# Performance work log

Hardware: AMD Instinct MI355X
Metric: run time of the kernel (lower is better)

## Reference

```python
import jax, jax.numpy as jnp
import numpy as np

V, D, H_FF, NH, L = 32000, 1024, 4096, 16, 4
HD = D // NH  # 64
B, T = 2, 2048
EPS = 1e-6
ROPE_BASE = 10000.0


def setup_inputs() -> dict:
    key = jax.random.key(0)
    ks = jax.random.split(key, 16)
    s = 0.02
    inp = {
        "idx": jax.random.randint(ks[0], (B, T), 0, V, dtype=jnp.int32),
        "targets": jax.random.randint(ks[1], (B, T), 0, V, dtype=jnp.int32),
        "embed": jax.random.normal(ks[2], (V, D), jnp.float32) * s,
        "wq": jax.random.normal(ks[3], (L, D, D), jnp.float32) * s,
        "wk": jax.random.normal(ks[4], (L, D, D), jnp.float32) * s,
        "wv": jax.random.normal(ks[5], (L, D, D), jnp.float32) * s,
        "wo": jax.random.normal(ks[6], (L, D, D), jnp.float32) * s,
        "w_gate": jax.random.normal(ks[7], (L, D, H_FF), jnp.float32) * s,
        "w_up": jax.random.normal(ks[8], (L, D, H_FF), jnp.float32) * s,
        "w_down": jax.random.normal(ks[9], (L, H_FF, D), jnp.float32) * s,
        "attn_norm": jnp.ones((L, D), jnp.float32),
        "mlp_norm": jnp.ones((L, D), jnp.float32),
        "final_norm": jnp.ones((D,), jnp.float32),
        "lm_head": jax.random.normal(ks[10], (V, D), jnp.float32) * s,
    }
    return inp


def rms_norm(x, w):
    var = jnp.mean(jnp.square(x), axis=-1, keepdims=True)
    return x * jax.lax.rsqrt(var + EPS) * w


def make_rope(t_len, hd):
    inv_freq = 1.0 / (ROPE_BASE ** (jnp.arange(0, hd, 2, dtype=jnp.float32) / hd))
    angles = jnp.arange(t_len, dtype=jnp.float32)[:, None] * inv_freq[None, :]  # [T, HD/2]
    return jnp.cos(angles), jnp.sin(angles)


def apply_rope(x, cos, sin):
    # x: [B, T, NH, HD]; half-split rotation (HF Llama style)
    x1, x2 = jnp.split(x, 2, axis=-1)
    c = cos[None, :, None, :]
    s = sin[None, :, None, :]
    return jnp.concatenate([x1 * c - x2 * s, x2 * c + x1 * s], axis=-1)


def forward(idx, targets, embed, wq, wk, wv, wo, w_gate, w_up, w_down,
            attn_norm, mlp_norm, final_norm, lm_head):
    b, t_len = idx.shape
    x = embed[idx]  # [B, T, D]
    cos, sin = make_rope(t_len, HD)
    causal = jnp.tril(jnp.ones((t_len, t_len), dtype=bool))
    scale = 1.0 / np.sqrt(HD)
    for l in range(L):
        # attention
        h = rms_norm(x, attn_norm[l])
        q = (h @ wq[l]).reshape(b, t_len, NH, HD)
        k = (h @ wk[l]).reshape(b, t_len, NH, HD)
        v = (h @ wv[l]).reshape(b, t_len, NH, HD)
        q = apply_rope(q, cos, sin)
        k = apply_rope(k, cos, sin)
        scores = jnp.einsum('bqhd,bkhd->bhqk', q, k) * scale
        scores = jnp.where(causal[None, None], scores, -jnp.inf)
        attn = jax.nn.softmax(scores, axis=-1)
        o = jnp.einsum('bhqk,bkhd->bqhd', attn, v).reshape(b, t_len, D)
        x = x + o @ wo[l]
        # SwiGLU MLP
        h = rms_norm(x, mlp_norm[l])
        x = x + (jax.nn.silu(h @ w_gate[l]) * (h @ w_up[l])) @ w_down[l]
    x = rms_norm(x, final_norm)
    logits = jnp.einsum('btd,vd->btv', x, lm_head)  # [B, T, V]
    logp = jax.nn.log_softmax(logits, axis=-1)
    nll = -jnp.take_along_axis(logp, targets[..., None], axis=-1)[..., 0]
    loss = jnp.mean(nll)
    return logits, loss


def reference(idx, targets, embed, wq, wk, wv, wo, w_gate, w_up, w_down,
              attn_norm, mlp_norm, final_norm, lm_head):
    return forward(idx, targets, embed, wq, wk, wv, wo, w_gate, w_up, w_down,
                   attn_norm, mlp_norm, final_norm, lm_head)
```

## Files before the change

kernel.cpp:

```cpp
#include <hip/hip_runtime.h>

typedef __attribute__((ext_vector_type(8))) short short8;
typedef __attribute__((ext_vector_type(4))) float f32x4;
typedef __attribute__((ext_vector_type(8))) unsigned short u16x8;
typedef unsigned short u16;

#define V_SIZE 32000
#define D_MODEL 1024
#define HFF 4096
#define NHEAD 16
#define HDIM 64
#define NLAYER 4
#define BT 4096
#define TSEQ 2048
#define QKV_STRIDE 3072
#define GU_STRIDE 8192

__device__ __forceinline__ u16 f2bf(float f) {
  union { float f; unsigned u; } v; v.f = f;
  unsigned r = v.u + 0x7fffu + ((v.u >> 16) & 1u);
  return (u16)(r >> 16);
}
__device__ __forceinline__ float bf2f(u16 h) {
  union { unsigned u; float f; } v; v.u = ((unsigned)h) << 16;
  return v.f;
}

__device__ __forceinline__ void gload_lds16(const void* g, void* l) {
  __builtin_amdgcn_global_load_lds((__attribute__((address_space(1))) void*)g,
                                   (__attribute__((address_space(3))) void*)l, 16, 0, 0);
}


__global__ void rope_table_kernel(float* __restrict__ cosb, float* __restrict__ sinb) {
  int i = blockIdx.x * 256 + threadIdx.x;
  int t = i >> 5, fi = i & 31;
  float freq = exp2f(-(2.0f * (float)fi / 64.0f) * log2f(10000.0f));
  float ang = (float)t * freq;
  cosb[i] = cosf(ang);
  sinb[i] = sinf(ang);
}

__global__ void convert_bf16_kernel(const float* __restrict__ src, u16* __restrict__ dst,
                                    const float* __restrict__ fn, long n8) {
  long i = (long)blockIdx.x * 256 + threadIdx.x;
  long stride = (long)gridDim.x * 256;
  for (; i < n8; i += stride) {
    const float4* s = (const float4*)(src + i * 8);
    float4 a = s[0], b = s[1];
    int k0 = (int)((i * 8) & (D_MODEL - 1));
    u16x8 r;
    r[0] = f2bf(a.x * fn[k0 + 0]); r[1] = f2bf(a.y * fn[k0 + 1]);
    r[2] = f2bf(a.z * fn[k0 + 2]); r[3] = f2bf(a.w * fn[k0 + 3]);
    r[4] = f2bf(b.x * fn[k0 + 4]); r[5] = f2bf(b.y * fn[k0 + 5]);
    r[6] = f2bf(b.z * fn[k0 + 6]); r[7] = f2bf(b.w * fn[k0 + 7]);
    *(u16x8*)(dst + i * 8) = r;
  }
}

__global__ __launch_bounds__(256) void transpose_bf16_kernel(const float* __restrict__ src0,
                                                             u16* __restrict__ dst0, int R, int C,
                                                             long srcStride, long dstStride,
                                                             int rowMode,
                                                             const float* __restrict__ nw0,
                                                             int nwStride) {
  __shared__ float tile[32][33];
  const float* src = src0 + (size_t)blockIdx.z * srcStride;
  u16* dst = dst0 + (size_t)blockIdx.z * dstStride;
  const float* nw = nw0 ? nw0 + (size_t)blockIdx.z * nwStride : nullptr;
  int tx = threadIdx.x & 31, ty = threadIdx.x >> 5;
  int bx = blockIdx.x, by = blockIdx.y;
#pragma unroll
  for (int i = 0; i < 32; i += 8) {
    int r = by * 32 + ty + i, c = bx * 32 + tx;
    tile[ty + i][tx] = src[(size_t)r * C + c];
  }
  __syncthreads();
#pragma unroll
  for (int i = 0; i < 32; i += 8) {
    int c = bx * 32 + ty + i;
    int r = by * 32 + tx;
    float val = tile[tx][ty + i];
    if (nw) val *= nw[r];
    int drow = c;
    if (rowMode == 1) drow = ((c >> 6) << 7) | (c & 63);
    else if (rowMode == 2) drow = ((c >> 6) << 7) | 64 | (c & 63);
    dst[(size_t)drow * R + r] = f2bf(val);
  }
}

__global__ __launch_bounds__(256) void embed_gather_kernel(const int* __restrict__ idx,
                                                           const float* __restrict__ embed,
                                                           float* __restrict__ x,
                                                           u16* __restrict__ xb,
                                                           float* __restrict__ rinv) {
  int t = blockIdx.x;
  int id = idx[t];
  float4 v = ((const float4*)embed)[(size_t)id * 256 + threadIdx.x];
  ((float4*)x)[(size_t)t * 256 + threadIdx.x] = v;
  u16* hp = xb + (size_t)t * D_MODEL + threadIdx.x * 4;
  hp[0] = f2bf(v.x); hp[1] = f2bf(v.y); hp[2] = f2bf(v.z); hp[3] = f2bf(v.w);
  float ss = v.x * v.x + v.y * v.y + v.z * v.z + v.w * v.w;
#pragma unroll
  for (int m = 32; m > 0; m >>= 1) ss += __shfl_xor(ss, m, 64);
  __shared__ float wsum[4];
  if ((threadIdx.x & 63) == 0) wsum[threadIdx.x >> 6] = ss;
  __syncthreads();
  if (threadIdx.x == 0) {
    float tot = wsum[0] + wsum[1] + wsum[2] + wsum[3];
    rinv[t] = rsqrtf(tot * (1.0f / (float)D_MODEL) + 1e-6f);
  }
}

__global__ void rinv_kernel(const float* __restrict__ ssqPart, float* __restrict__ rinv) {
  int r = blockIdx.x * 256 + threadIdx.x;
  float s = 0.f;
#pragma unroll
  for (int i = 0; i < 16; i++) s += ssqPart[(size_t)r * 16 + i];
  rinv[r] = rsqrtf(s * (1.0f / (float)D_MODEL) + 1e-6f);
}

__global__ void scale_xb_kernel(const u16* __restrict__ xb, const float* __restrict__ rinv,
                                u16* __restrict__ xbf) {
  long i = (long)blockIdx.x * 256 + threadIdx.x;
  int row = (int)(i >> 7);
  float ri = rinv[row];
  short8 v = *(const short8*)(xb + i * 8);
  u16x8 r;
#pragma unroll
  for (int j = 0; j < 8; j++) r[j] = f2bf(bf2f((u16)v[j]) * ri);
  *(u16x8*)(xbf + i * 8) = r;
}

__global__ __launch_bounds__(256) void vtrans_kernel(const u16* __restrict__ qkv,
                                                     u16* __restrict__ vt) {
  __shared__ u16 lds[64 * 64];
  const int tid = threadIdx.x;
  const int bh = blockIdx.y, tt = blockIdx.x;
  const int b = bh >> 4, h = bh & 15;
  const int tok0 = b * TSEQ + tt * 64;
  const int hoff = 2 * D_MODEL + h * HDIM;
#pragma unroll
  for (int it = 0; it < 2; it++) {
    int idx = it * 256 + tid;
    int row = idx >> 3, c = (idx & 7) * 8;
    short8 v = *(const short8*)(qkv + (size_t)(tok0 + row) * QKV_STRIDE + hoff + c);
    *(short8*)&lds[row * 64 + (c ^ ((row & 7) << 3))] = v;
  }
  __syncthreads();
#pragma unroll
  for (int it = 0; it < 2; it++) {
    int idx = it * 256 + tid;
    int d = idx >> 3, t0 = (idx & 7) * 8;
    u16x8 pk;
#pragma unroll
    for (int j = 0; j < 8; j++) {
      int t = t0 + j;
      pk[j] = lds[t * 64 + (((d & ~7) ^ ((t & 7) << 3)) | (d & 7))];
    }
    *(u16x8*)(vt + ((size_t)bh * 64 + d) * TSEQ + tt * 64 + t0) = pk;
  }
}

template <int EPI>
__global__ __launch_bounds__(256, 4) void gemm128_kernel(const u16* __restrict__ A,
                                                         const u16* __restrict__ B, void* Cp,
                                                         float* __restrict__ partM,
                                                         float* __restrict__ partS,
                                                         const float* __restrict__ cosb,
                                                         const float* __restrict__ sinb,
                                                         const float* __restrict__ rinv,
                                                         int M, int N, int K, int chunkBn) {
  __shared__ __align__(16) u16 smem_ab[2][128 * 64];
  u16* As = smem_ab[0];
  u16* Bs = smem_ab[1];
  const int tid = threadIdx.x;
  const int lane = tid & 63, wid = tid >> 6;
  const int wr = wid >> 1, wc = wid & 1;
  const int q = lane >> 4, l15 = lane & 15;
  const int nbm = M >> 7;
  const int nbmx = nbm >> 3;
  const int cs = nbm * chunkBn;
  const int chunk = (int)blockIdx.x / cs;
  const int r0 = (int)blockIdx.x - chunk * cs;
  const int s2 = r0 >> 3;
  const int bm = (r0 & 7) * nbmx + (s2 % nbmx);
  const int bn = chunk * chunkBn + (s2 / nbmx);
  const size_t abase = (size_t)bm * 128 * K;
  const size_t bbase = (size_t)bn * 128 * K;
  f32x4 acc[4][4] = {};
  for (int k0 = 0; k0 < K; k0 += 64) {
#pragma unroll
    for (int i = 0; i < 4; i++) {
      int idx8 = i * 256 + tid;
      int row = idx8 >> 3, ch = idx8 & 7;
      int sc = (ch ^ (row & 7)) << 3;
      gload_lds16(A + abase + (size_t)row * K + k0 + sc, As + idx8 * 8);
      gload_lds16(B + bbase + (size_t)row * K + k0 + sc, Bs + idx8 * 8);
    }
    __syncthreads();
#pragma unroll
    for (int ks = 0; ks < 2; ks++) {
      short8 af[4], bfr[4];
      int chunkc = ks * 4 + q;
#pragma unroll
      for (int mi = 0; mi < 4; mi++) {
        int row = wr * 64 + mi * 16 + l15;
        af[mi] = *(const short8*)&As[row * 64 + ((chunkc ^ (row & 7)) << 3)];
      }
#pragma unroll
      for (int ni = 0; ni < 4; ni++) {
        int row = wc * 64 + ni * 16 + l15;
        bfr[ni] = *(const short8*)&Bs[row * 64 + ((chunkc ^ (row & 7)) << 3)];
      }
#pragma unroll
      for (int mi = 0; mi < 4; mi++)
#pragma unroll
        for (int ni = 0; ni < 4; ni++)
          acc[mi][ni] = __builtin_amdgcn_mfma_f32_16x16x32_bf16(af[mi], bfr[ni], acc[mi][ni], 0, 0, 0);
    }
    __syncthreads();
  }

  if (EPI == 5) {
    float* upf = (float*)&smem_ab[0][0];
    if (wc == 1) {
#pragma unroll
      for (int mi = 0; mi < 4; mi++)
#pragma unroll
        for (int ni = 0; ni < 4; ni++)
#pragma unroll
          for (int j = 0; j < 4; j++) {
            int r = wr * 64 + mi * 16 + q * 4 + j;
            int cswz = (ni ^ ((r >> 2) & 3)) * 16 + l15;
            upf[r * 64 + cswz] = acc[mi][ni][j];
          }
    }
    __syncthreads();
    if (wc == 0) {
#pragma unroll
      for (int mi = 0; mi < 4; mi++)
#pragma unroll
        for (int j = 0; j < 4; j++) {
          int rloc = wr * 64 + mi * 16 + q * 4 + j;
          int rr = bm * 128 + rloc;
          float ri = rinv[rr];
#pragma unroll
          for (int ni = 0; ni < 4; ni++) {
            int cswz = (ni ^ ((rloc >> 2) & 3)) * 16 + l15;
            float g = acc[mi][ni][j] * ri;
            float u = upf[rloc * 64 + cswz] * ri;
            float rsl = g / (1.0f + expf(-g)) * u;
            ((u16*)Cp)[(size_t)rr * (N >> 1) + bn * 64 + ni * 16 + l15] = f2bf(rsl);
          }
        }
    }
    return;
  }

#pragma unroll
  for (int mi = 0; mi < 4; mi++)
#pragma unroll
    for (int j = 0; j < 4; j++) {
      int rr = bm * 128 + wr * 64 + mi * 16 + q * 4 + j;
      float vv[4];
      if (EPI == 4) {
        float ri = rinv[rr];
#pragma unroll
        for (int ni = 0; ni < 4; ni++) vv[ni] = acc[mi][ni][j] * ri;
      } else {
#pragma unroll
        for (int ni = 0; ni < 4; ni++) vv[ni] = acc[mi][ni][j];
      }
      if (EPI == 0) {
        float mx = fmaxf(fmaxf(vv[0], vv[1]), fmaxf(vv[2], vv[3]));
        mx = fmaxf(mx, __shfl_xor(mx, 1, 64));
        mx = fmaxf(mx, __shfl_xor(mx, 2, 64));
        mx = fmaxf(mx, __shfl_xor(mx, 4, 64));
        mx = fmaxf(mx, __shfl_xor(mx, 8, 64));
        float sm = 0.f;
#pragma unroll
        for (int ni = 0; ni < 4; ni++) sm += expf(vv[ni] - mx);
        sm += __shfl_xor(sm, 1, 64);
        sm += __shfl_xor(sm, 2, 64);
        sm += __shfl_xor(sm, 4, 64);
        sm += __shfl_xor(sm, 8, 64);
        if (l15 == 0) {
          int nt = (N >> 6);
          partM[(size_t)rr * nt + (bn << 1) + wc] = mx;
          partS[(size_t)rr * nt + (bn << 1) + wc] = sm;
        }
      }
      if (EPI == 4) {
        if (((bn << 1) + wc) < 32) {
          int t = rr & (TSEQ - 1);
#pragma unroll
          for (int ni = 0; ni < 2; ni++) {
            int fi = ni * 16 + l15;
            float c = cosb[t * 32 + fi], s = sinb[t * 32 + fi];
            float x1 = vv[ni], x2 = vv[ni + 2];
            vv[ni] = x1 * c - x2 * s;
            vv[ni + 2] = x2 * c + x1 * s;
          }
        }
      }
#pragma unroll
      for (int ni = 0; ni < 4; ni++) {
        int cn = bn * 128 + wc * 64 + ni * 16 + l15;
        size_t off = (size_t)rr * N + cn;
        if (EPI == 0) __builtin_nontemporal_store(vv[ni], (float*)Cp + off);
        else ((u16*)Cp)[off] = f2bf(vv[ni]);
      }
    }
}

__global__ __launch_bounds__(256, 4) void gemm64_kernel(const u16* __restrict__ A,
                                                        const u16* __restrict__ B, float* __restrict__ Cp,
                                                        const float* __restrict__ resid,
                                                        u16* __restrict__ xbout,
                                                        float* __restrict__ ssqPart,
                                                        int M, int N, int K) {
  __shared__ __align__(16) u16 As[64 * 64];
  __shared__ __align__(16) u16 Bs[128 * 64];
  const int tid = threadIdx.x;
  const int lane = tid & 63, wid = tid >> 6;
  const int wr = wid >> 1, wc = wid & 1;
  const int q = lane >> 4, l15 = lane & 15;
  const int nbm = M >> 6;
  const int nbmx = nbm >> 3;
  const int s2 = (int)blockIdx.x >> 3;
  const int bm = ((int)blockIdx.x & 7) * nbmx + (s2 % nbmx);
  const int bn = s2 / nbmx;
  const size_t abase = (size_t)bm * 64 * K;
  const size_t bbase = (size_t)bn * 128 * K;
  f32x4 acc[2][4] = {};
  for (int k0 = 0; k0 < K; k0 += 64) {
#pragma unroll
    for (int i = 0; i < 2; i++) {
      int idx8 = i * 256 + tid;
      int row = idx8 >> 3, ch = idx8 & 7;
      int sc = (ch ^ (row & 7)) << 3;
      gload_lds16(A + abase + (size_t)row * K + k0 + sc, As + idx8 * 8);
    }
#pragma unroll
    for (int i = 0; i < 4; i++) {
      int idx8 = i * 256 + tid;
      int row = idx8 >> 3, ch = idx8 & 7;
      int sc = (ch ^ (row & 7)) << 3;
      gload_lds16(B + bbase + (size_t)row * K + k0 + sc, Bs + idx8 * 8);
    }
    __syncthreads();
#pragma unroll
    for (int ks = 0; ks < 2; ks++) {
      short8 af[2], bfr[4];
      int chunkc = ks * 4 + q;
#pragma unroll
      for (int mi = 0; mi < 2; mi++) {
        int row = wr * 32 + mi * 16 + l15;
        af[mi] = *(const short8*)&As[row * 64 + ((chunkc ^ (row & 7)) << 3)];
      }
#pragma unroll
      for (int ni = 0; ni < 4; ni++) {
        int row = wc * 64 + ni * 16 + l15;
        bfr[ni] = *(const short8*)&Bs[row * 64 + ((chunkc ^ (row & 7)) << 3)];
      }
#pragma unroll
      for (int mi = 0; mi < 2; mi++)
#pragma unroll
        for (int ni = 0; ni < 4; ni++)
          acc[mi][ni] = __builtin_amdgcn_mfma_f32_16x16x32_bf16(af[mi], bfr[ni], acc[mi][ni], 0, 0, 0);
    }
    __syncthreads();
  }
#pragma unroll
  for (int mi = 0; mi < 2; mi++)
#pragma unroll
    for (int j = 0; j < 4; j++) {
      int rr = bm * 64 + wr * 32 + mi * 16 + q * 4 + j;
      float ssq = 0.f;
#pragma unroll
      for (int ni = 0; ni < 4; ni++) {
        int cn = bn * 128 + wc * 64 + ni * 16 + l15;
        size_t off = (size_t)rr * N + cn;
        float nx = resid[off] + acc[mi][ni][j];
        Cp[off] = nx;
        xbout[off] = f2bf(nx);
        ssq += nx * nx;
      }
      ssq += __shfl_xor(ssq, 1, 64);
      ssq += __shfl_xor(ssq, 2, 64);
      ssq += __shfl_xor(ssq, 4, 64);
      ssq += __shfl_xor(ssq, 8, 64);
      if (l15 == 0) ssqPart[(size_t)rr * 16 + (bn << 1) + wc] = ssq;
    }
}

__global__ __launch_bounds__(256) void attn_kernel(const u16* __restrict__ qkv,
                                                   const u16* __restrict__ vt,
                                                   u16* __restrict__ o) {
  __shared__ __align__(16) u16 Ks[64 * 64];
  __shared__ __align__(16) u16 Vt[64 * 64];
  __shared__ u16 Ps[4][16 * 64];
  const u16* q = qkv;
  const u16* k = qkv + D_MODEL;
  const int tid = threadIdx.x, lane = tid & 63, wid = tid >> 6;
  const int qg = lane >> 4, l15 = lane & 15;
  const int bh = blockIdx.y;
  const int b = bh >> 4, h = bh & 15;
  const int tok0 = b * TSEQ;
  const int hoff = h * HDIM;
  const u16* vtb = vt + (size_t)bh * 64 * TSEQ;

  for (int half = 0; half < 2; half++) {
    const int qt = half == 0 ? (int)blockIdx.x : 31 - (int)blockIdx.x;
    const int qrow0 = qt * 64 + wid * 16;

    short8 aq[2];
#pragma unroll
    for (int ks = 0; ks < 2; ks++) {
      int r = qrow0 + l15;
      int d = ks * 32 + qg * 8;
      aq[ks] = *(const short8*)(q + (size_t)(tok0 + r) * QKV_STRIDE + hoff + d);
    }
    f32x4 oacc[4] = {};
    float mrow[4], lrow[4];
#pragma unroll
    for (int j = 0; j < 4; j++) { mrow[j] = -1e30f; lrow[j] = 0.f; }

    const int nkt = qt + 1;
    for (int kt = 0; kt < nkt; kt++) {
      const int kv0 = kt * 64;
#pragma unroll
      for (int it = 0; it < 2; it++) {
        int idx = it * 256 + tid;
        int row = idx >> 3, ch = idx & 7;
        int sc = (ch ^ (row & 7)) << 3;
        gload_lds16(k + (size_t)(tok0 + kv0 + row) * QKV_STRIDE + hoff + sc, Ks + idx * 8);
        gload_lds16(vtb + (size_t)row * TSEQ + kv0 + sc, Vt + idx * 8);
      }
      __syncthreads();
      f32x4 sc[4] = {};
#pragma unroll
      for (int ks = 0; ks < 2; ks++) {
        short8 bk[4];
        int kcol = ks * 32 + qg * 8;
#pragma unroll
        for (int ni = 0; ni < 4; ni++) {
          int r = ni * 16 + l15;
          bk[ni] = *(const short8*)&Ks[r * 64 + (kcol ^ ((r & 7) << 3))];
        }
#pragma unroll
        for (int ni = 0; ni < 4; ni++)
          sc[ni] = __builtin_amdgcn_mfma_f32_16x16x32_bf16(aq[ks], bk[ni], sc[ni], 0, 0, 0);
      }
      float pm[4];
#pragma unroll
      for (int j = 0; j < 4; j++) pm[j] = -1e30f;
#pragma unroll
      for (int ni = 0; ni < 4; ni++)
#pragma unroll
        for (int j = 0; j < 4; j++) {
          int rq = qrow0 + qg * 4 + j;
          int ck = kv0 + ni * 16 + l15;
          float s = sc[ni][j] * 0.125f;
          if (ck > rq) s = -1e30f;
          sc[ni][j] = s;
          pm[j] = fmaxf(pm[j], s);
        }
#pragma unroll
      for (int j = 0; j < 4; j++) {
        float t = pm[j];
        t = fmaxf(t, __shfl_xor(t, 1, 64));
        t = fmaxf(t, __shfl_xor(t, 2, 64));
        t = fmaxf(t, __shfl_xor(t, 4, 64));
        t = fmaxf(t, __shfl_xor(t, 8, 64));
        pm[j] = t;
      }
#pragma unroll
      for (int j = 0; j < 4; j++) {
        float mn = fmaxf(mrow[j], pm[j]);
        float fac = expf(mrow[j] - mn);
        lrow[j] *= fac;
#pragma unroll
        for (int df = 0; df < 4; df++) oacc[df][j] *= fac;
        mrow[j] = mn;
      }
      float psum[4] = {};
#pragma unroll
      for (int ni = 0; ni < 4; ni++)
#pragma unroll
        for (int j = 0; j < 4; j++) {
          float p = expf(sc[ni][j] - mrow[j]);
          psum[j] += p;
          int r16 = qg * 4 + j;
          int cc = ni * 16 + l15;
          Ps[wid][r16 * 64 + (cc ^ ((r16 & 7) << 3))] = f2bf(p);
        }
#pragma unroll
      for (int j = 0; j < 4; j++) {
        float t = psum[j];
        t += __shfl_xor(t, 1, 64);
        t += __shfl_xor(t, 2, 64);
        t += __shfl_xor(t, 4, 64);
        t += __shfl_xor(t, 8, 64);
        lrow[j] += t;
      }
#pragma unroll
      for (int kf = 0; kf < 2; kf++) {
        short8 pa, bv[4];
        int kcol = kf * 32 + qg * 8;
        {
          int r = l15;
          pa = *(const short8*)&Ps[wid][r * 64 + (kcol ^ ((r & 7) << 3))];
        }
#pragma unroll
        for (int df = 0; df < 4; df++) {
          int r = df * 16 + l15;
          bv[df] = *(const short8*)&Vt[r * 64 + (kcol ^ ((r & 7) << 3))];
        }
#pragma unroll
        for (int df = 0; df < 4; df++)
          oacc[df] = __builtin_amdgcn_mfma_f32_16x16x32_bf16(pa, bv[df], oacc[df], 0, 0, 0);
      }
      __syncthreads();
    }
#pragma unroll
    for (int df = 0; df < 4; df++)
#pragma unroll
      for (int j = 0; j < 4; j++) {
        int r = qrow0 + qg * 4 + j;
        int d = df * 16 + l15;
        float val = oacc[df][j] / lrow[j];
        o[(size_t)(tok0 + r) * D_MODEL + hoff + d] = f2bf(val);
      }
  }
}


__global__ void nll_finalize_kernel(const float* __restrict__ partM, const float* __restrict__ partS,
                                    const float* __restrict__ logits, const int* __restrict__ targets,
                                    float* __restrict__ nll) {
  int tok = blockIdx.x;
  int lane = threadIdx.x;
  const int NTL = V_SIZE >> 6;
  float m = -1e30f, s = 0.f;
  for (int i = lane; i < NTL; i += 64) {
    float m2 = partM[(size_t)tok * NTL + i];
    float s2 = partS[(size_t)tok * NTL + i];
    float nm = fmaxf(m, m2);
    s = s * expf(m - nm) + s2 * expf(m2 - nm);
    m = nm;
  }
#pragma unroll
  for (int mask = 1; mask < 64; mask <<= 1) {
    float m2 = __shfl_xor(m, mask, 64);
    float s2 = __shfl_xor(s, mask, 64);
    float nm = fmaxf(m, m2);
    s = s * expf(m - nm) + s2 * expf(m2 - nm);
    m = nm;
  }
  if (lane == 0)
    nll[tok] = m + logf(s) - logits[(size_t)tok * V_SIZE + targets[tok]];
}

__global__ void loss_reduce_kernel(const float* __restrict__ nll, float* __restrict__ out) {
  float s = 0.f;
  for (int i = threadIdx.x; i < BT; i += 256) s += nll[i];
#pragma unroll
  for (int mask = 1; mask < 64; mask <<= 1) s += __shfl_xor(s, mask, 64);
  __shared__ float sm[4];
  if ((threadIdx.x & 63) == 0) sm[threadIdx.x >> 6] = s;
  __syncthreads();
  if (threadIdx.x == 0) out[0] = (sm[0] + sm[1] + sm[2] + sm[3]) / (float)BT;
}


extern "C" void kernel_launch(void* const* d_in, const int* in_sizes, int n_in,
                              void* d_out, int out_size, void* d_ws, size_t ws_size,
                              hipStream_t stream) {
  const int* idx = (const int*)d_in[0];
  const int* targets = (const int*)d_in[1];
  const float* embed = (const float*)d_in[2];
  const float* wq = (const float*)d_in[3];
  const float* wk = (const float*)d_in[4];
  const float* wv = (const float*)d_in[5];
  const float* wo = (const float*)d_in[6];
  const float* w_gate = (const float*)d_in[7];
  const float* w_up = (const float*)d_in[8];
  const float* w_down = (const float*)d_in[9];
  const float* attn_norm = (const float*)d_in[10];
  const float* mlp_norm = (const float*)d_in[11];
  const float* final_norm = (const float*)d_in[12];
  const float* lm_head = (const float*)d_in[13];
  float* out = (float*)d_out;

  char* ws = (char*)d_ws;
  size_t off = 0;
  auto alloc = [&](size_t bytes) {
    void* p = ws + off;
    off += (bytes + 255) & ~(size_t)255;
    return p;
  };
  const size_t DD = (size_t)D_MODEL * D_MODEL;
  float* rope_cos = (float*)alloc((size_t)TSEQ * 32 * 4);
  float* rope_sin = (float*)alloc((size_t)TSEQ * 32 * 4);
  float* X = (float*)alloc((size_t)BT * D_MODEL * 4);
  u16* Xb = (u16*)alloc((size_t)BT * D_MODEL * 2);
  u16* XbF = (u16*)alloc((size_t)BT * D_MODEL * 2);
  float* Rinv = (float*)alloc((size_t)BT * 4);
  float* SsqP = (float*)alloc((size_t)BT * 16 * 4);
  u16* QKVb = (u16*)alloc((size_t)BT * QKV_STRIDE * 2);
  u16* Vtb = (u16*)alloc((size_t)32 * 64 * TSEQ * 2);
  u16* Ob = (u16*)alloc((size_t)BT * D_MODEL * 2);
  u16* Gb = (u16*)alloc((size_t)BT * HFF * 2);
  u16* WQKVT = (u16*)alloc((size_t)NLAYER * QKV_STRIDE * D_MODEL * 2);
  u16* WOT = (u16*)alloc((size_t)NLAYER * DD * 2);
  u16* WGU = (u16*)alloc((size_t)NLAYER * GU_STRIDE * D_MODEL * 2);
  u16* WDT = (u16*)alloc((size_t)NLAYER * D_MODEL * HFF * 2);
  u16* LMH = (u16*)alloc((size_t)V_SIZE * D_MODEL * 2);
  float* NLLb = (float*)alloc((size_t)BT * 4);
  float* PartM = (float*)alloc((size_t)BT * (V_SIZE >> 6) * 4);
  float* PartS = (float*)alloc((size_t)BT * (V_SIZE >> 6) * 4);

  rope_table_kernel<<<256, 256, 0, stream>>>(rope_cos, rope_sin);
  convert_bf16_kernel<<<4096, 256, 0, stream>>>(lm_head, LMH, final_norm, (long)V_SIZE * D_MODEL / 8);
  embed_gather_kernel<<<BT, 256, 0, stream>>>(idx, embed, X, Xb, Rinv);

  const long QKVW = (long)QKV_STRIDE * D_MODEL;
  const long GUW = (long)GU_STRIDE * D_MODEL;
  const long DW = (long)D_MODEL * HFF;
  transpose_bf16_kernel<<<dim3(32, 32, NLAYER), 256, 0, stream>>>(wq, WQKVT, D_MODEL, D_MODEL, DD, QKVW, 0, attn_norm, D_MODEL);
  transpose_bf16_kernel<<<dim3(32, 32, NLAYER), 256, 0, stream>>>(wk, WQKVT + DD, D_MODEL, D_MODEL, DD, QKVW, 0, attn_norm, D_MODEL);
  transpose_bf16_kernel<<<dim3(32, 32, NLAYER), 256, 0, stream>>>(wv, WQKVT + 2 * DD, D_MODEL, D_MODEL, DD, QKVW, 0, attn_norm, D_MODEL);
  transpose_bf16_kernel<<<dim3(32, 32, NLAYER), 256, 0, stream>>>(wo, WOT, D_MODEL, D_MODEL, DD, DD, 0, nullptr, 0);
  transpose_bf16_kernel<<<dim3(128, 32, NLAYER), 256, 0, stream>>>(w_gate, WGU, D_MODEL, HFF, DW, GUW, 1, mlp_norm, D_MODEL);
  transpose_bf16_kernel<<<dim3(128, 32, NLAYER), 256, 0, stream>>>(w_up, WGU, D_MODEL, HFF, DW, GUW, 2, mlp_norm, D_MODEL);
  transpose_bf16_kernel<<<dim3(32, 128, NLAYER), 256, 0, stream>>>(w_down, WDT, HFF, D_MODEL, DW, DW, 0, nullptr, 0);

  for (int l = 0; l < NLAYER; l++) {
    gemm128_kernel<4><<<(QKV_STRIDE / 128) * (BT / 128), 256, 0, stream>>>(
        Xb, WQKVT + (size_t)l * QKVW, QKVb, nullptr, nullptr, rope_cos, rope_sin,
        Rinv, BT, QKV_STRIDE, D_MODEL, QKV_STRIDE / 128);
    vtrans_kernel<<<dim3(32, 32), 256, 0, stream>>>(QKVb, Vtb);
    attn_kernel<<<dim3(16, 32), 256, 0, stream>>>(QKVb, Vtb, Ob);
    gemm64_kernel<<<(BT / 64) * (D_MODEL / 128), 256, 0, stream>>>(
        Ob, WOT + (size_t)l * DD, X, X, Xb, SsqP, BT, D_MODEL, D_MODEL);
    rinv_kernel<<<BT / 256, 256, 0, stream>>>(SsqP, Rinv);

    gemm128_kernel<5><<<(GU_STRIDE / 128) * (BT / 128), 256, 0, stream>>>(
        Xb, WGU + (size_t)l * GUW, Gb, nullptr, nullptr, nullptr, nullptr,
        Rinv, BT, GU_STRIDE, D_MODEL, 32);
    gemm64_kernel<<<(BT / 64) * (D_MODEL / 128), 256, 0, stream>>>(
        Gb, WDT + (size_t)l * DW, X, X, Xb, SsqP, BT, D_MODEL, HFF);
    rinv_kernel<<<BT / 256, 256, 0, stream>>>(SsqP, Rinv);
  }

  scale_xb_kernel<<<BT * D_MODEL / (256 * 8), 256, 0, stream>>>(Xb, Rinv, XbF);
  gemm128_kernel<0><<<(V_SIZE / 128) * (BT / 128), 256, 0, stream>>>(
      XbF, LMH, out, PartM, PartS, nullptr, nullptr,
      nullptr, BT, V_SIZE, D_MODEL, 50);
  nll_finalize_kernel<<<BT, 64, 0, stream>>>(PartM, PartS, out, targets, NLLb);
  loss_reduce_kernel<<<1, 256, 0, stream>>>(NLLb, out + (size_t)BT * V_SIZE);
}
```

Before: 1.737 ms.

## Keep residual stream in bf16 and fold attention scale into Q projection

Removes the fp32 residual buffer X: the embed gather and residual GEMM epilogues now read and write only the bf16 Xb copy, so each residual GEMM avoids an fp32 read and write. The softmax scale and log2(e) are folded into the Q columns in the QKV epilogue, which lets attention use exp2f. Causal masking now runs only on the diagonal tile. Keeping the residual in bf16 adds rounding error that accumulates across layers and may threaten accuracy tolerance.

Measured after the change: 1.649 ms. 5.1% less time.

```diff
diff --git a/kernel.cpp b/kernel.cpp
--- a/kernel.cpp
+++ b/kernel.cpp
@@ -15,6 +15,7 @@
 #define TSEQ 2048
 #define QKV_STRIDE 3072
 #define GU_STRIDE 8192
+#define QSCALE 0.18033688011112043f
 
 __device__ __forceinline__ u16 f2bf(float f) {
   union { float f; unsigned u; } v; v.f = f;
@@ -91,13 +92,11 @@
 
 __global__ __launch_bounds__(256) void embed_gather_kernel(const int* __restrict__ idx,
                                                            const float* __restrict__ embed,
-                                                           float* __restrict__ x,
                                                            u16* __restrict__ xb,
                                                            float* __restrict__ rinv) {
   int t = blockIdx.x;
   int id = idx[t];
   float4 v = ((const float4*)embed)[(size_t)id * 256 + threadIdx.x];
-  ((float4*)x)[(size_t)t * 256 + threadIdx.x] = v;
   u16* hp = xb + (size_t)t * D_MODEL + threadIdx.x * 4;
   hp[0] = f2bf(v.x); hp[1] = f2bf(v.y); hp[2] = f2bf(v.z); hp[3] = f2bf(v.w);
   float ss = v.x * v.x + v.y * v.y + v.z * v.z + v.w * v.w;
@@ -266,6 +265,7 @@
       float vv[4];
       if (EPI == 4) {
         float ri = rinv[rr];
+        if (((bn << 1) + wc) < 16) ri *= QSCALE;
 #pragma unroll
         for (int ni = 0; ni < 4; ni++) vv[ni] = acc[mi][ni][j] * ri;
       } else {
@@ -315,8 +315,8 @@
 }
 
 __global__ __launch_bounds__(256, 4) void gemm64_kernel(const u16* __restrict__ A,
-                                                        const u16* __restrict__ B, float* __restrict__ Cp,
-                                                        const float* __restrict__ resid,
+                                                        const u16* __restrict__ B,
+                                                        const u16* __restrict__ resid,
                                                         u16* __restrict__ xbout,
                                                         float* __restrict__ ssqPart,
                                                         int M, int N, int K) {
@@ -382,8 +382,7 @@
       for (int ni = 0; ni < 4; ni++) {
         int cn = bn * 128 + wc * 64 + ni * 16 + l15;
         size_t off = (size_t)rr * N + cn;
-        float nx = resid[off] + acc[mi][ni][j];
-        Cp[off] = nx;
+        float nx = bf2f(resid[off]) + acc[mi][ni][j];
         xbout[off] = f2bf(nx);
         ssq += nx * nx;
       }
@@ -456,17 +455,24 @@
       float pm[4];
 #pragma unroll
       for (int j = 0; j < 4; j++) pm[j] = -1e30f;
-#pragma unroll
-      for (int ni = 0; ni < 4; ni++)
-#pragma unroll
-        for (int j = 0; j < 4; j++) {
-          int rq = qrow0 + qg * 4 + j;
-          int ck = kv0 + ni * 16 + l15;
-          float s = sc[ni][j] * 0.125f;
-          if (ck > rq) s = -1e30f;
-          sc[ni][j] = s;
-          pm[j] = fmaxf(pm[j], s);
-        }
+      if (kt == qt) {
+#pragma unroll
+        for (int ni = 0; ni < 4; ni++)
+#pragma unroll
+          for (int j = 0; j < 4; j++) {
+            int rq = qrow0 + qg * 4 + j;
+            int ck = kv0 + ni * 16 + l15;
+            float s = sc[ni][j];
+            if (ck > rq) s = -1e30f;
+            sc[ni][j] = s;
+            pm[j] = fmaxf(pm[j], s);
+          }
+      } else {
+#pragma unroll
+        for (int ni = 0; ni < 4; ni++)
+#pragma unroll
+          for (int j = 0; j < 4; j++) pm[j] = fmaxf(pm[j], sc[ni][j]);
+      }
 #pragma unroll
       for (int j = 0; j < 4; j++) {
         float t = pm[j];
@@ -479,7 +485,7 @@
 #pragma unroll
       for (int j = 0; j < 4; j++) {
         float mn = fmaxf(mrow[j], pm[j]);
-        float fac = expf(mrow[j] - mn);
+        float fac = exp2f(mrow[j] - mn);
         lrow[j] *= fac;
 #pragma unroll
         for (int df = 0; df < 4; df++) oacc[df][j] *= fac;
@@ -490,7 +496,7 @@
       for (int ni = 0; ni < 4; ni++)
 #pragma unroll
         for (int j = 0; j < 4; j++) {
-          float p = expf(sc[ni][j] - mrow[j]);
+          float p = exp2f(sc[ni][j] - mrow[j]);
           psum[j] += p;
           int r16 = qg * 4 + j;
           int cc = ni * 16 + l15;
@@ -604,7 +610,6 @@
   const size_t DD = (size_t)D_MODEL * D_MODEL;
   float* rope_cos = (float*)alloc((size_t)TSEQ * 32 * 4);
   float* rope_sin = (float*)alloc((size_t)TSEQ * 32 * 4);
-  float* X = (float*)alloc((size_t)BT * D_MODEL * 4);
   u16* Xb = (u16*)alloc((size_t)BT * D_MODEL * 2);
   u16* XbF = (u16*)alloc((size_t)BT * D_MODEL * 2);
   float* Rinv = (float*)alloc((size_t)BT * 4);
@@ -624,7 +629,7 @@
 
   rope_table_kernel<<<256, 256, 0, stream>>>(rope_cos, rope_sin);
   convert_bf16_kernel<<<4096, 256, 0, stream>>>(lm_head, LMH, final_norm, (long)V_SIZE * D_MODEL / 8);
-  embed_gather_kernel<<<BT, 256, 0, stream>>>(idx, embed, X, Xb, Rinv);
+  embed_gather_kernel<<<BT, 256, 0, stream>>>(idx, embed, Xb, Rinv);
 
   const long QKVW = (long)QKV_STRIDE * D_MODEL;
   const long GUW = (long)GU_STRIDE * D_MODEL;
@@ -644,14 +649,14 @@
     vtrans_kernel<<<dim3(32, 32), 256, 0, stream>>>(QKVb, Vtb);
     attn_kernel<<<dim3(16, 32), 256, 0, stream>>>(QKVb, Vtb, Ob);
     gemm64_kernel<<<(BT / 64) * (D_MODEL / 128), 256, 0, stream>>>(
-        Ob, WOT + (size_t)l * DD, X, X, Xb, SsqP, BT, D_MODEL, D_MODEL);
+        Ob, WOT + (size_t)l * DD, Xb, Xb, SsqP, BT, D_MODEL, D_MODEL);
     rinv_kernel<<<BT / 256, 256, 0, stream>>>(SsqP, Rinv);
 
     gemm128_kernel<5><<<(GU_STRIDE / 128) * (BT / 128), 256, 0, stream>>>(
         Xb, WGU + (size_t)l * GUW, Gb, nullptr, nullptr, nullptr, nullptr,
         Rinv, BT, GU_STRIDE, D_MODEL, 32);
     gemm64_kernel<<<(BT / 64) * (D_MODEL / 128), 256, 0, stream>>>(
-        Gb, WDT + (size_t)l * DW, X, X, Xb, SsqP, BT, D_MODEL, HFF);
+        Gb, WDT + (size_t)l * DW, Xb, Xb, SsqP, BT, D_MODEL, HFF);
     rinv_kernel<<<BT / 256, 256, 0, stream>>>(SsqP, Rinv);
   }
 
```
